# Optimization experiments

Measured on AMD Instinct MI355X. Metric: run time of the kernel, lower is better.

The kernel has to match this reference:

```python
import jax, jax.numpy as jnp
import numpy as np

D_MODEL, D_HEAD, N_HEAD = 1024, 64, 16
B, S = 8, 1024


def setup_inputs() -> dict:
    key = jax.random.key(0)
    ks = jax.random.split(key, 11)
    sc = 1.0 / np.sqrt(D_MODEL)
    inp = {
        "query": jax.random.normal(ks[0], (B, S, D_MODEL), jnp.float32),
        "key": jax.random.normal(ks[1], (B, S, D_MODEL), jnp.float32),
        "value": jax.random.normal(ks[2], (B, S, D_MODEL), jnp.float32),
        # stacked per-head Q/K projections: [H, d_model, d_head]
        "Wq": jax.random.normal(ks[3], (N_HEAD, D_MODEL, D_HEAD), jnp.float32) * sc,
        "bq": jax.random.normal(ks[4], (N_HEAD, D_HEAD), jnp.float32) * 0.01,
        "Wk": jax.random.normal(ks[5], (N_HEAD, D_MODEL, D_HEAD), jnp.float32) * sc,
        "bk": jax.random.normal(ks[6], (N_HEAD, D_HEAD), jnp.float32) * 0.01,
        # shared V projection
        "Wv": jax.random.normal(ks[7], (D_MODEL, D_HEAD), jnp.float32) * sc,
        "bv": jax.random.normal(ks[8], (D_HEAD,), jnp.float32) * 0.01,
        # output projection d_head -> d_model
        "Wo": jax.random.normal(ks[9], (D_HEAD, D_MODEL), jnp.float32) * (1.0 / np.sqrt(D_HEAD)),
        "bo": jax.random.normal(ks[10], (D_MODEL,), jnp.float32) * 0.01,
    }
    return inp


def reference(query, key, value, Wq, bq, Wk, bk, Wv, bv, Wo, bo):
    scale = D_HEAD ** -0.5
    # per-head projections, batched over heads: [B, H, S, d_head]
    Q = jnp.einsum("bsd,hdk->bhsk", query, Wq) + bq[None, :, None, :]
    K = jnp.einsum("bsd,hdk->bhsk", key, Wk) + bk[None, :, None, :]
    # shared V: [B, S, d_head]
    V = value @ Wv + bv
    # attention weights per head: [B, H, S, S]
    wei = jax.nn.softmax(jnp.einsum("bhsk,bhtk->bhst", Q, K) * scale, axis=-1)
    # head outputs averaged (shared V): [B, S, d_head]
    out = jnp.mean(jnp.einsum("bhst,btk->bhsk", wei, V), axis=1)
    return out @ Wo + bo
```

## Files before the change

kernel.cpp:

```cpp
#include <hip/hip_runtime.h>
#include <hip/hip_bf16.h>
#include <math.h>

typedef __attribute__((ext_vector_type(4))) float  f32x4;
typedef __attribute__((ext_vector_type(8))) __bf16 bf16x8;
typedef __attribute__((ext_vector_type(4))) __bf16 bf16x4;
typedef __attribute__((ext_vector_type(4))) short  s16x4;

#define SCL 0.18033688011111543f
#define MFMA16(a, b, c)   __builtin_amdgcn_mfma_f32_16x16x32_bf16((a), (b), (c), 0, 0, 0)
#define MFMA16K16(a, b, c) __builtin_amdgcn_mfma_f32_16x16x16bf16_1k((a), (b), (c), 0, 0, 0)

union B4 { bf16x4 b; s16x4 s; };

__device__ __forceinline__ float exp2_fast(float x) {
    float r;
    asm("v_exp_f32 %0, %1" : "=v"(r) : "v"(x));
    return r;
}

__global__ __launch_bounds__(256) void pack_qk(
    const float* __restrict__ Wq, const float* __restrict__ Wk,
    __bf16* __restrict__ WqT, __bf16* __restrict__ WkT)
{
    __shared__ __bf16 T0[64][68];
    __shared__ __bf16 T1[64][68];
    const int tid = threadIdx.x;
    const int h = blockIdx.x & 15, kt = blockIdx.x >> 4;
    const int kk = tid >> 2, cf = (tid & 3) * 16;
    const size_t base = (size_t)h * 65536 + (size_t)(kt * 64 + kk) * 64 + cf;
    #pragma unroll
    for (int j = 0; j < 4; ++j) {
        f32x4 v = *(const f32x4*)&Wq[base + 4 * j];
        f32x4 u = *(const f32x4*)&Wk[base + 4 * j];
        bf16x4 vb, ub;
        #pragma unroll
        for (int e = 0; e < 4; ++e) { vb[e] = (__bf16)v[e]; ub[e] = (__bf16)u[e]; }
        *(bf16x4*)&T0[kk][cf + 4 * j] = vb;
        *(bf16x4*)&T1[kk][cf + 4 * j] = ub;
    }
    __syncthreads();
    const int c = tid >> 2, k8 = (tid & 3) * 16;
    bf16x8 q0, q1, k0v, k1v;
    #pragma unroll
    for (int j = 0; j < 8; ++j) {
        q0[j] = T0[k8 + j][c];     q1[j] = T0[k8 + 8 + j][c];
        k0v[j] = T1[k8 + j][c];    k1v[j] = T1[k8 + 8 + j][c];
    }
    size_t dst = (size_t)(h * 64 + c) * 1024 + kt * 64 + k8;
    *(bf16x8*)&WqT[dst] = q0;  *(bf16x8*)&WqT[dst + 8] = q1;
    *(bf16x8*)&WkT[dst] = k0v; *(bf16x8*)&WkT[dst + 8] = k1v;
}

__global__ __launch_bounds__(256) void pack_misc(
    const float* __restrict__ Wv, const float* __restrict__ bv,
    const float* __restrict__ Wo,
    __bf16* __restrict__ WvT, float* __restrict__ bvP, __bf16* __restrict__ WoT)
{
    int idx = blockIdx.x * 256 + threadIdx.x;
    if (idx < 131072) {
        int n = idx >> 10, k = idx & 1023;
        WvT[idx] = (n < 64) ? (__bf16)Wv[k * 64 + n] : (__bf16)0.0f;
    }
    if (idx < 65536) {
        int n = idx >> 6, d = idx & 63;
        WoT[idx] = (__bf16)Wo[d * 1024 + n];
    }
    if (idx < 128) bvP[idx] = (idx < 64) ? bv[idx] : 0.0f;
}

__global__ __launch_bounds__(512, 2) void proj_gemm_f32(
    const float* __restrict__ A, const __bf16* __restrict__ Bt,
    const float* __restrict__ bias, __bf16* __restrict__ C, float oscale)
{
    __shared__ __bf16 As[2][128][36];
    __shared__ __bf16 Bs[2][256][36];

    const int tid = threadIdx.x;
    const int lane = tid & 63, w = tid >> 6;
    const int wr = w >> 2, wc = w & 3;
    const int l15 = lane & 15, g = lane >> 4;
    const int m0 = blockIdx.x * 128, n0 = blockIdx.y * 256;
    const int arow = tid >> 2, acf = (tid & 3) * 8;
    const int brow = tid >> 1, bcf = (tid & 1) * 16;

    f32x4 areg[2];
    bf16x8 breg[2];
    #pragma unroll
    for (int j = 0; j < 2; ++j) {
        areg[j] = *(const f32x4*)&A[(size_t)(m0 + arow) * 1024 + acf + 4 * j];
        breg[j] = *(const bf16x8*)&Bt[(size_t)(n0 + brow) * 1024 + bcf + 8 * j];
    }

    f32x4 acc[4][4] = {};
    int cur = 0;
    for (int k0 = 0; k0 < 1024; k0 += 32) {
        #pragma unroll
        for (int j = 0; j < 2; ++j) {
            bf16x4 c4;
            #pragma unroll
            for (int e = 0; e < 4; ++e) c4[e] = (__bf16)areg[j][e];
            *(bf16x4*)&As[cur][arow][acf + 4 * j] = c4;
            *(bf16x8*)&Bs[cur][brow][bcf + 8 * j] = breg[j];
        }
        if (k0 < 992) {
            #pragma unroll
            for (int j = 0; j < 2; ++j) {
                areg[j] = *(const f32x4*)&A[(size_t)(m0 + arow) * 1024 + k0 + 32 + acf + 4 * j];
                breg[j] = *(const bf16x8*)&Bt[(size_t)(n0 + brow) * 1024 + k0 + 32 + bcf + 8 * j];
            }
        }
        __syncthreads();
        __builtin_amdgcn_s_setprio(1);
        bf16x8 af[4], bfv[4];
        #pragma unroll
        for (int mi = 0; mi < 4; ++mi)
            af[mi] = *(const bf16x8*)&As[cur][64 * wr + 16 * mi + l15][8 * g];
        #pragma unroll
        for (int ni = 0; ni < 4; ++ni)
            bfv[ni] = *(const bf16x8*)&Bs[cur][64 * wc + 16 * ni + l15][8 * g];
        #pragma unroll
        for (int mi = 0; mi < 4; ++mi)
            #pragma unroll
            for (int ni = 0; ni < 4; ++ni)
                acc[mi][ni] = MFMA16(af[mi], bfv[ni], acc[mi][ni]);
        __builtin_amdgcn_s_setprio(0);
        cur ^= 1;
    }

    #pragma unroll
    for (int mi = 0; mi < 4; ++mi)
        #pragma unroll
        for (int ni = 0; ni < 4; ++ni) {
            int n = n0 + 64 * wc + 16 * ni + l15;
            float bn = bias[n];
            #pragma unroll
            for (int r = 0; r < 4; ++r) {
                int m = m0 + 64 * wr + 16 * mi + 4 * g + r;
                C[(size_t)m * 1024 + n] = (__bf16)((acc[mi][ni][r] + bn) * oscale);
            }
        }
}

__global__ __launch_bounds__(256, 2) void proj_v(
    const float* __restrict__ A, const __bf16* __restrict__ Bt,
    const float* __restrict__ bias, __bf16* __restrict__ C)
{
    __shared__ __bf16 As[2][64][72];
    __shared__ __bf16 Bs[2][64][72];

    const int tid = threadIdx.x;
    const int lane = tid & 63, w = tid >> 6;
    const int wr = w >> 1, wc = w & 1;
    const int l15 = lane & 15, g = lane >> 4;
    const int m0 = blockIdx.x * 64;
    const int arow = tid >> 2, acf = (tid & 3) * 16;
    const int bcf = (tid & 3) * 16;

    f32x4 areg[4];
    bf16x8 breg[2];
    #pragma unroll
    for (int j = 0; j < 4; ++j)
        areg[j] = *(const f32x4*)&A[(size_t)(m0 + arow) * 1024 + acf + 4 * j];
    #pragma unroll
    for (int j = 0; j < 2; ++j)
        breg[j] = *(const bf16x8*)&Bt[(size_t)arow * 1024 + bcf + 8 * j];

    f32x4 acc[2][2] = {};
    int cur = 0;
    for (int k0 = 0; k0 < 1024; k0 += 64) {
        #pragma unroll
        for (int j = 0; j < 4; ++j) {
            bf16x4 c4;
            #pragma unroll
            for (int e = 0; e < 4; ++e) c4[e] = (__bf16)areg[j][e];
            *(bf16x4*)&As[cur][arow][acf + 4 * j] = c4;
        }
        #pragma unroll
        for (int j = 0; j < 2; ++j)
            *(bf16x8*)&Bs[cur][arow][bcf + 8 * j] = breg[j];
        if (k0 < 960) {
            #pragma unroll
            for (int j = 0; j < 4; ++j)
                areg[j] = *(const f32x4*)&A[(size_t)(m0 + arow) * 1024 + k0 + 64 + acf + 4 * j];
            #pragma unroll
            for (int j = 0; j < 2; ++j)
                breg[j] = *(const bf16x8*)&Bt[(size_t)arow * 1024 + k0 + 64 + bcf + 8 * j];
        }
        __syncthreads();
        #pragma unroll
        for (int ks = 0; ks < 2; ++ks) {
            bf16x8 af[2], bfv[2];
            #pragma unroll
            for (int mi = 0; mi < 2; ++mi)
                af[mi] = *(const bf16x8*)&As[cur][32 * wr + 16 * mi + l15][32 * ks + 8 * g];
            #pragma unroll
            for (int ni = 0; ni < 2; ++ni)
                bfv[ni] = *(const bf16x8*)&Bs[cur][32 * wc + 16 * ni + l15][32 * ks + 8 * g];
            #pragma unroll
            for (int mi = 0; mi < 2; ++mi)
                #pragma unroll
                for (int ni = 0; ni < 2; ++ni)
                    acc[mi][ni] = MFMA16(af[mi], bfv[ni], acc[mi][ni]);
        }
        __syncthreads();
        cur ^= 1;
    }

    #pragma unroll
    for (int mi = 0; mi < 2; ++mi)
        #pragma unroll
        for (int ni = 0; ni < 2; ++ni) {
            int n = 32 * wc + 16 * ni + l15;
            float bn = bias[n];
            #pragma unroll
            for (int r = 0; r < 4; ++r) {
                int m = m0 + 32 * wr + 16 * mi + 4 * g + r;
                C[(size_t)n * 8192 + m] = (__bf16)(acc[mi][ni][r] + bn);
            }
        }
}

__global__ __launch_bounds__(128, 4) void attn_kernel(
    const __bf16* __restrict__ Qb, const __bf16* __restrict__ Kb,
    const __bf16* __restrict__ Vt, __bf16* __restrict__ Oh)
{
    __shared__ __bf16 Ks[2][32][68];
    __shared__ __bf16 Vs[2][64][44];

    const int qt = blockIdx.x, bh = blockIdx.y;
    const int b = bh >> 4, h = bh & 15;
    const int tid = threadIdx.x;
    const int lane = tid & 63, w = tid >> 6;
    const int l15 = lane & 15, g = lane >> 4;
    const int s0 = b * 1024 + qt * 64;

    const int krow = tid >> 2, kc = (tid & 3) * 16;
    const int vrow = tid >> 1, vc = (tid & 1) * 16;

    bf16x8 qf[2][2];
    #pragma unroll
    for (int mi = 0; mi < 2; ++mi)
        #pragma unroll
        for (int ks = 0; ks < 2; ++ks)
            qf[mi][ks] = *(const bf16x8*)
                &Qb[(size_t)(s0 + 32 * w + 16 * mi + l15) * 1024 + h * 64 + 32 * ks + 8 * g];

    const __bf16* Kbase = Kb + (size_t)(b * 1024) * 1024 + h * 64;
    const __bf16* Vbase = Vt + (size_t)b * 1024;

    bf16x8 kreg[2], vreg[2];
    #pragma unroll
    for (int j = 0; j < 2; ++j) {
        kreg[j] = *(const bf16x8*)&Kbase[(size_t)krow * 1024 + kc + 8 * j];
        vreg[j] = *(const bf16x8*)&Vbase[(size_t)vrow * 8192 + vc + 8 * j];
    }

    f32x4 acc_o[2][4] = {};
    float l_par[2] = {0.0f, 0.0f};

    int cur = 0;
    for (int it = 0; it < 32; ++it) {
        *(bf16x8*)&Ks[cur][krow][kc]     = kreg[0];
        *(bf16x8*)&Ks[cur][krow][kc + 8] = kreg[1];
        *(bf16x8*)&Vs[cur][vrow][vc]     = vreg[0];
        *(bf16x8*)&Vs[cur][vrow][vc + 8] = vreg[1];
        if (it < 31) {
            int t1 = (it + 1) * 32;
            #pragma unroll
            for (int j = 0; j < 2; ++j) {
                kreg[j] = *(const bf16x8*)&Kbase[(size_t)(t1 + krow) * 1024 + kc + 8 * j];
                vreg[j] = *(const bf16x8*)&Vbase[(size_t)vrow * 8192 + t1 + vc + 8 * j];
            }
        }
        __syncthreads();

        f32x4 pacc[2][2] = {};
        __builtin_amdgcn_s_setprio(1);
        #pragma unroll
        for (int ks = 0; ks < 2; ++ks) {
            bf16x8 kf[2];
            #pragma unroll
            for (int ni = 0; ni < 2; ++ni)
                kf[ni] = *(const bf16x8*)&Ks[cur][16 * ni + l15][32 * ks + 8 * g];
            #pragma unroll
            for (int mi = 0; mi < 2; ++mi)
                #pragma unroll
                for (int ni = 0; ni < 2; ++ni)
                    pacc[mi][ni] = MFMA16(kf[ni], qf[mi][ks], pacc[mi][ni]);
        }
        __builtin_amdgcn_s_setprio(0);

        s16x4 pb[2][2];
        #pragma unroll
        for (int mi = 0; mi < 2; ++mi) {
            float rs = 0.0f;
            #pragma unroll
            for (int ni = 0; ni < 2; ++ni) {
                B4 pk;
                #pragma unroll
                for (int r = 0; r < 4; ++r) {
                    float pv = exp2_fast(pacc[mi][ni][r]);
                    rs += pv;
                    pk.b[r] = (__bf16)pv;
                }
                pb[mi][ni] = pk.s;
            }
            l_par[mi] += rs;
        }

        __builtin_amdgcn_s_setprio(1);
        #pragma unroll
        for (int c = 0; c < 2; ++c) {
            s16x4 vf[4];
            #pragma unroll
            for (int nd = 0; nd < 4; ++nd) {
                B4 vv;
                vv.b = *(const bf16x4*)&Vs[cur][16 * nd + l15][16 * c + 4 * g];
                vf[nd] = vv.s;
            }
            #pragma unroll
            for (int mi = 0; mi < 2; ++mi)
                #pragma unroll
                for (int nd = 0; nd < 4; ++nd)
                    acc_o[mi][nd] = MFMA16K16(vf[nd], pb[mi][c], acc_o[mi][nd]);
        }
        __builtin_amdgcn_s_setprio(0);
        cur ^= 1;
    }

    #pragma unroll
    for (int mi = 0; mi < 2; ++mi) {
        float l = l_par[mi];
        l += __shfl_xor(l, 16);
        l += __shfl_xor(l, 32);
        float rl = 1.0f / l;
        int q = qt * 64 + 32 * w + 16 * mi + l15;
        #pragma unroll
        for (int nd = 0; nd < 4; ++nd) {
            bf16x4 ov;
            #pragma unroll
            for (int r = 0; r < 4; ++r) ov[r] = (__bf16)(acc_o[mi][nd][r] * rl);
            *(bf16x4*)&Oh[(size_t)(bh * 1024 + q) * 64 + 16 * nd + 4 * g] = ov;
        }
    }
}

__global__ __launch_bounds__(256) void mean_kernel(
    const __bf16* __restrict__ Oh, __bf16* __restrict__ Om)
{
    int idx = blockIdx.x * 256 + threadIdx.x;
    int m = idx >> 3, d8 = (idx & 7) * 8;
    int b = m >> 10, q = m & 1023;
    const __bf16* src = Oh + (size_t)(b * 16) * 65536 + (size_t)q * 64 + d8;
    float s[8] = {};
    #pragma unroll
    for (int h = 0; h < 16; ++h) {
        bf16x8 v = *(const bf16x8*)&src[(size_t)h * 65536];
        #pragma unroll
        for (int j = 0; j < 8; ++j) s[j] += (float)v[j];
    }
    bf16x8 o;
    #pragma unroll
    for (int j = 0; j < 8; ++j) o[j] = (__bf16)(s[j] * 0.0625f);
    *(bf16x8*)&Om[(size_t)m * 64 + d8] = o;
}

__global__ __launch_bounds__(256, 4) void out_gemm(
    const __bf16* __restrict__ Om, const __bf16* __restrict__ WoT,
    const float* __restrict__ bo, float* __restrict__ out)
{
    const int tid = threadIdx.x;
    const int lane = tid & 63, w = tid >> 6;
    const int wr = w >> 1, wc = w & 1;
    const int l15 = lane & 15, g = lane >> 4;
    const int m0 = blockIdx.x * 128, n0 = blockIdx.y * 128;

    f32x4 acc[4][4] = {};
    #pragma unroll
    for (int ks = 0; ks < 2; ++ks) {
        bf16x8 af[4], bfv[4];
        #pragma unroll
        for (int mi = 0; mi < 4; ++mi)
            af[mi] = *(const bf16x8*)&Om[(size_t)(m0 + 64 * wr + 16 * mi + l15) * 64 + 32 * ks + 8 * g];
        #pragma unroll
        for (int ni = 0; ni < 4; ++ni)
            bfv[ni] = *(const bf16x8*)&WoT[(size_t)(n0 + 64 * wc + 16 * ni + l15) * 64 + 32 * ks + 8 * g];
        #pragma unroll
        for (int mi = 0; mi < 4; ++mi)
            #pragma unroll
            for (int ni = 0; ni < 4; ++ni)
                acc[mi][ni] = MFMA16(af[mi], bfv[ni], acc[mi][ni]);
    }
    #pragma unroll
    for (int mi = 0; mi < 4; ++mi)
        #pragma unroll
        for (int ni = 0; ni < 4; ++ni) {
            int n = n0 + 64 * wc + 16 * ni + l15;
            float bn = bo[n];
            #pragma unroll
            for (int r = 0; r < 4; ++r) {
                int m = m0 + 64 * wr + 16 * mi + 4 * g + r;
                out[(size_t)m * 1024 + n] = acc[mi][ni][r] + bn;
            }
        }
}

extern "C" void kernel_launch(void* const* d_in, const int* in_sizes, int n_in,
                              void* d_out, int out_size, void* d_ws, size_t ws_size,
                              hipStream_t stream)
{
    const float* query = (const float*)d_in[0];
    const float* key_  = (const float*)d_in[1];
    const float* value = (const float*)d_in[2];
    const float* Wq = (const float*)d_in[3];
    const float* bq = (const float*)d_in[4];
    const float* Wk = (const float*)d_in[5];
    const float* bk = (const float*)d_in[6];
    const float* Wv = (const float*)d_in[7];
    const float* bv = (const float*)d_in[8];
    const float* Wo = (const float*)d_in[9];
    const float* bo = (const float*)d_in[10];
    float* out = (float*)d_out;

    char* p = (char*)d_ws;
    __bf16* Qbuf = (__bf16*)p; p += 8192ull * 1024 * 2;
    __bf16* Kbuf = (__bf16*)p; p += 8192ull * 1024 * 2;
    __bf16* VtB  = (__bf16*)p; p += 64ull * 8192 * 2;
    __bf16* WqT  = (__bf16*)p; p += 1024ull * 1024 * 2;
    __bf16* WkT  = (__bf16*)p; p += 1024ull * 1024 * 2;
    __bf16* WvT  = (__bf16*)p; p += 128ull * 1024 * 2;
    __bf16* WoT  = (__bf16*)p; p += 1024ull * 64 * 2;
    float*  bvP  = (float*)p;  p += 128 * 4;
    __bf16* Oh   = (__bf16*)p; p += 8ull * 16 * 1024 * 64 * 2;
    __bf16* Om   = (__bf16*)p; p += 8192ull * 64 * 2;

    pack_qk<<<256, 256, 0, stream>>>(Wq, Wk, WqT, WkT);
    pack_misc<<<512, 256, 0, stream>>>(Wv, bv, Wo, WvT, bvP, WoT);
    proj_gemm_f32<<<dim3(64, 4), 512, 0, stream>>>(query, WqT, bq, Qbuf, SCL);
    proj_gemm_f32<<<dim3(64, 4), 512, 0, stream>>>(key_,  WkT, bk, Kbuf, 1.0f);
    proj_v<<<128, 256, 0, stream>>>(value, WvT, bvP, VtB);
    attn_kernel<<<dim3(16, 128), 128, 0, stream>>>(Qbuf, Kbuf, VtB, Oh);
    mean_kernel<<<256, 256, 0, stream>>>(Oh, Om);
    out_gemm<<<dim3(64, 8), 256, 0, stream>>>(Om, WoT, bo, out);
}
```

Measured before the change: 143.7 us.

## Retile Q/K projection GEMM to 128x128 with K-step 64, merge pack kernels

The Q/K projection GEMM moves from 128x256 tiles with a K-step of 32 to 128x128 tiles with a K-step of 64. This doubles the grid to 512 blocks, which should improve CU occupancy and halve the number of barriers per K loop. In exchange, each output tile now re-reads the fp32 A operand from global memory more often. The two weight-packing kernels are merged into one launch to save launch overhead, and the attention V shared-memory padding changes from 44 to 46, likely to reduce bank conflicts.

```diff
diff --git a/kernel.cpp b/kernel.cpp
--- a/kernel.cpp
+++ b/kernel.cpp
@@ -19,13 +19,29 @@
     return r;
 }
 
-__global__ __launch_bounds__(256) void pack_qk(
+__global__ __launch_bounds__(256) void pack_all(
     const float* __restrict__ Wq, const float* __restrict__ Wk,
-    __bf16* __restrict__ WqT, __bf16* __restrict__ WkT)
-{
+    const float* __restrict__ Wv, const float* __restrict__ bv,
+    const float* __restrict__ Wo,
+    __bf16* __restrict__ WqT, __bf16* __restrict__ WkT,
+    __bf16* __restrict__ WvT, float* __restrict__ bvP, __bf16* __restrict__ WoT)
+{
+    const int tid = threadIdx.x;
+    if (blockIdx.x >= 256) {
+        int idx = (blockIdx.x - 256) * 256 + tid;
+        if (idx < 131072) {
+            int n = idx >> 10, k = idx & 1023;
+            WvT[idx] = (n < 64) ? (__bf16)Wv[k * 64 + n] : (__bf16)0.0f;
+        }
+        if (idx < 65536) {
+            int n = idx >> 6, d = idx & 63;
+            WoT[idx] = (__bf16)Wo[d * 1024 + n];
+        }
+        if (idx < 128) bvP[idx] = (idx < 64) ? bv[idx] : 0.0f;
+        return;
+    }
     __shared__ __bf16 T0[64][68];
     __shared__ __bf16 T1[64][68];
-    const int tid = threadIdx.x;
     const int h = blockIdx.x & 15, kt = blockIdx.x >> 4;
     const int kk = tid >> 2, cf = (tid & 3) * 16;
     const size_t base = (size_t)h * 65536 + (size_t)(kt * 64 + kk) * 64 + cf;
@@ -52,91 +68,80 @@
     *(bf16x8*)&WkT[dst] = k0v; *(bf16x8*)&WkT[dst + 8] = k1v;
 }
 
-__global__ __launch_bounds__(256) void pack_misc(
-    const float* __restrict__ Wv, const float* __restrict__ bv,
-    const float* __restrict__ Wo,
-    __bf16* __restrict__ WvT, float* __restrict__ bvP, __bf16* __restrict__ WoT)
-{
-    int idx = blockIdx.x * 256 + threadIdx.x;
-    if (idx < 131072) {
-        int n = idx >> 10, k = idx & 1023;
-        WvT[idx] = (n < 64) ? (__bf16)Wv[k * 64 + n] : (__bf16)0.0f;
-    }
-    if (idx < 65536) {
-        int n = idx >> 6, d = idx & 63;
-        WoT[idx] = (__bf16)Wo[d * 1024 + n];
-    }
-    if (idx < 128) bvP[idx] = (idx < 64) ? bv[idx] : 0.0f;
-}
-
 __global__ __launch_bounds__(512, 2) void proj_gemm_f32(
     const float* __restrict__ A, const __bf16* __restrict__ Bt,
     const float* __restrict__ bias, __bf16* __restrict__ C, float oscale)
 {
-    __shared__ __bf16 As[2][128][36];
-    __shared__ __bf16 Bs[2][256][36];
+    __shared__ __bf16 As[2][128][68];
+    __shared__ __bf16 Bs[2][128][68];
 
     const int tid = threadIdx.x;
     const int lane = tid & 63, w = tid >> 6;
-    const int wr = w >> 2, wc = w & 3;
+    const int wr = w >> 1, wc = w & 1;
     const int l15 = lane & 15, g = lane >> 4;
-    const int m0 = blockIdx.x * 128, n0 = blockIdx.y * 256;
-    const int arow = tid >> 2, acf = (tid & 3) * 8;
-    const int brow = tid >> 1, bcf = (tid & 1) * 16;
-
-    f32x4 areg[2];
+    const int m0 = blockIdx.x * 128, n0 = blockIdx.y * 128;
+    const int srow = tid >> 2, scf = (tid & 3) * 16;
+
+    f32x4 areg[4];
     bf16x8 breg[2];
     #pragma unroll
-    for (int j = 0; j < 2; ++j) {
-        areg[j] = *(const f32x4*)&A[(size_t)(m0 + arow) * 1024 + acf + 4 * j];
-        breg[j] = *(const bf16x8*)&Bt[(size_t)(n0 + brow) * 1024 + bcf + 8 * j];
-    }
-
-    f32x4 acc[4][4] = {};
+    for (int j = 0; j < 4; ++j)
+        areg[j] = *(const f32x4*)&A[(size_t)(m0 + srow) * 1024 + scf + 4 * j];
+    #pragma unroll
+    for (int j = 0; j < 2; ++j)
+        breg[j] = *(const bf16x8*)&Bt[(size_t)(n0 + srow) * 1024 + scf + 8 * j];
+
+    f32x4 acc[2][4] = {};
     int cur = 0;
-    for (int k0 = 0; k0 < 1024; k0 += 32) {
-        #pragma unroll
-        for (int j = 0; j < 2; ++j) {
+    for (int k0 = 0; k0 < 1024; k0 += 64) {
+        #pragma unroll
+        for (int j = 0; j < 4; ++j) {
             bf16x4 c4;
             #pragma unroll
             for (int e = 0; e < 4; ++e) c4[e] = (__bf16)areg[j][e];
-            *(bf16x4*)&As[cur][arow][acf + 4 * j] = c4;
-            *(bf16x8*)&Bs[cur][brow][bcf + 8 * j] = breg[j];
-        }
-        if (k0 < 992) {
-            #pragma unroll
-            for (int j = 0; j < 2; ++j) {
-                areg[j] = *(const f32x4*)&A[(size_t)(m0 + arow) * 1024 + k0 + 32 + acf + 4 * j];
-                breg[j] = *(const bf16x8*)&Bt[(size_t)(n0 + brow) * 1024 + k0 + 32 + bcf + 8 * j];
-            }
+            *(bf16x4*)&As[cur][srow][scf + 4 * j] = c4;
+        }
+        #pragma unroll
+        for (int j = 0; j < 2; ++j)
+            *(bf16x8*)&Bs[cur][srow][scf + 8 * j] = breg[j];
+        if (k0 < 960) {
+            #pragma unroll
+            for (int j = 0; j < 4; ++j)
+                areg[j] = *(const f32x4*)&A[(size_t)(m0 + srow) * 1024 + k0 + 64 + scf + 4 * j];
+            #pragma unroll
+            for (int j = 0; j < 2; ++j)
+                breg[j] = *(const bf16x8*)&Bt[(size_t)(n0 + srow) * 1024 + k0 + 64 + scf + 8 * j];
         }
         __syncthreads();
         __builtin_amdgcn_s_setprio(1);
-        bf16x8 af[4], bfv[4];
-        #pragma unroll
-        for (int mi = 0; mi < 4; ++mi)
-            af[mi] = *(const bf16x8*)&As[cur][64 * wr + 16 * mi + l15][8 * g];
-        #pragma unroll
-        for (int ni = 0; ni < 4; ++ni)
-            bfv[ni] = *(const bf16x8*)&Bs[cur][64 * wc + 16 * ni + l15][8 * g];
-        #pragma unroll
-        for (int mi = 0; mi < 4; ++mi)
+        #pragma unroll
+        for (int ks = 0; ks < 2; ++ks) {
+            bf16x8 af[2], bfv[4];
+            #pragma unroll
+            for (int mi = 0; mi < 2; ++mi)
+                af[mi] = *(const bf16x8*)&As[cur][32 * wr + 16 * mi + l15][32 * ks + 8 * g];
             #pragma unroll
             for (int ni = 0; ni < 4; ++ni)
-                acc[mi][ni] = MFMA16(af[mi], bfv[ni], acc[mi][ni]);
+                bfv[ni] = *(const bf16x8*)&Bs[cur][64 * wc + 16 * ni + l15][32 * ks + 8 * g];
+            #pragma unroll
+            for (int mi = 0; mi < 2; ++mi)
+                #pragma unroll
+                for (int ni = 0; ni < 4; ++ni)
+                    acc[mi][ni] = MFMA16(af[mi], bfv[ni], acc[mi][ni]);
+        }
         __builtin_amdgcn_s_setprio(0);
         cur ^= 1;
     }
 
     #pragma unroll
-    for (int mi = 0; mi < 4; ++mi)
+    for (int mi = 0; mi < 2; ++mi)
         #pragma unroll
         for (int ni = 0; ni < 4; ++ni) {
             int n = n0 + 64 * wc + 16 * ni + l15;
             float bn = bias[n];
             #pragma unroll
             for (int r = 0; r < 4; ++r) {
-                int m = m0 + 64 * wr + 16 * mi + 4 * g + r;
+                int m = m0 + 32 * wr + 16 * mi + 4 * g + r;
                 C[(size_t)m * 1024 + n] = (__bf16)((acc[mi][ni][r] + bn) * oscale);
             }
         }
@@ -226,7 +231,7 @@
     const __bf16* __restrict__ Vt, __bf16* __restrict__ Oh)
 {
     __shared__ __bf16 Ks[2][32][68];
-    __shared__ __bf16 Vs[2][64][44];
+    __shared__ __bf16 Vs[2][64][46];
 
     const int qt = blockIdx.x, bh = blockIdx.y;
     const int b = bh >> 4, h = bh & 15;
@@ -435,10 +440,9 @@
     __bf16* Oh   = (__bf16*)p; p += 8ull * 16 * 1024 * 64 * 2;
     __bf16* Om   = (__bf16*)p; p += 8192ull * 64 * 2;
 
-    pack_qk<<<256, 256, 0, stream>>>(Wq, Wk, WqT, WkT);
-    pack_misc<<<512, 256, 0, stream>>>(Wv, bv, Wo, WvT, bvP, WoT);
-    proj_gemm_f32<<<dim3(64, 4), 512, 0, stream>>>(query, WqT, bq, Qbuf, SCL);
-    proj_gemm_f32<<<dim3(64, 4), 512, 0, stream>>>(key_,  WkT, bk, Kbuf, 1.0f);
+    pack_all<<<768, 256, 0, stream>>>(Wq, Wk, Wv, bv, Wo, WqT, WkT, WvT, bvP, WoT);
+    proj_gemm_f32<<<dim3(64, 8), 512, 0, stream>>>(query, WqT, bq, Qbuf, SCL);
+    proj_gemm_f32<<<dim3(64, 8), 512, 0, stream>>>(key_,  WkT, bk, Kbuf, 1.0f);
     proj_v<<<128, 256, 0, stream>>>(value, WvT, bvP, VtB);
     attn_kernel<<<dim3(16, 128), 128, 0, stream>>>(Qbuf, Kbuf, VtB, Oh);
     mean_kernel<<<256, 256, 0, stream>>>(Oh, Om);
```

Result: slower. 148.1 us (+3.0%).
